# Kernel optimization log

Hardware: AMD Instinct MI355X
Metric: run time of the kernel (lower is better)

## Reference

```python
import jax, jax.numpy as jnp
import numpy as np

# Dimensions (see shape_source)
IN_VEC = 131072          # input_vector_size
NUM_CAPS = 512           # num_capsules (output capsules)
CAP_SIZE = 256           # capsule_size
RF_SIZE = 64             # receptive_field_size
RF_PER_CAP = CAP_SIZE // RF_SIZE        # 4
IN_CAPS = IN_VEC // CAP_SIZE            # 512 input_eff_capsules
CONN_P = 0.1             # connection_probability


def setup_inputs() -> dict:
    key = jax.random.key(0)
    kx, kc, kw = jax.random.split(key, 3)
    x = jax.random.normal(kx, (IN_VEC,), dtype=jnp.float32)
    # Sparse ScRRAMBLe routing tensor: mostly zeros, gated by connection probability.
    # Shape (input_eff_capsules, rf_per_cap_in, num_capsules, rf_per_cap_out) per einsum 'ijkl,ijm->klm'.
    Ci = (jax.random.uniform(kc, (IN_CAPS, RF_PER_CAP, NUM_CAPS, RF_PER_CAP)) < CONN_P).astype(jnp.float32)
    # glorot_normal over last two axes: fan_in = fan_out = RF_SIZE -> std = sqrt(2/(64+64)) = 0.125
    glorot_std = float(np.sqrt(2.0 / (RF_SIZE + RF_SIZE)))
    Wi = glorot_std * jax.random.normal(kw, (NUM_CAPS, RF_PER_CAP, RF_PER_CAP, RF_SIZE, RF_SIZE), dtype=jnp.float32)
    return {"x": x, "Ci": Ci, "Wi": Wi}


def reference(x, Ci, Wi):
    # x: (IN_VEC,) -> (input_eff_capsules, rf_per_cap, rf_size)
    x_reshaped = x.reshape(IN_CAPS, RF_PER_CAP, RF_SIZE)
    # Route input receptive fields to output capsule slots:
    # x_routed: (num_capsules, rf_per_cap, rf_size)
    x_routed = jnp.einsum('ijkl,ijm->klm', Ci, x_reshaped)
    # Per-capsule small batched transform:
    # y: (num_capsules, rf_per_cap, rf_size)
    y = jnp.einsum('ijklm,ikm->ijl', Wi, x_routed)
    return y
```

## Files before the change

kernel.cpp:

```cpp
#include <hip/hip_runtime.h>


typedef float f4 __attribute__((ext_vector_type(4)));

#define NCH 4

__global__ __launch_bounds__(256) void route_kernel(
    const float* __restrict__ x,
    const float* __restrict__ Ci,
    float* __restrict__ xr_part)
{
    const int iq  = blockIdx.x;
    const int c   = blockIdx.y;
    const int t   = threadIdx.x;
    const int il  = t >> 6;
    const int g   = (t >> 4) & 3;
    const int mq4 = t & 15;
    const int i   = (iq << 2) + il;

    const f4* __restrict__ Ci4 = (const f4*)Ci;
    const f4* __restrict__ x4  = (const f4*)x;

    __shared__ f4 part[1024];

    f4 a0 = {0.f,0.f,0.f,0.f};
    f4 a1 = {0.f,0.f,0.f,0.f};
    f4 a2 = {0.f,0.f,0.f,0.f};
    f4 a3 = {0.f,0.f,0.f,0.f};

    const int ijpc = 2048 / NCH;
    const int sub  = ijpc >> 2;
    const int base = c * ijpc + g * sub;
    #pragma unroll 4
    for (int it = 0; it < sub; ++it) {
        const int ij = base + it;
        const f4 c4 = Ci4[ij * 512 + i];
        const f4 xv = x4[(ij << 4) + mq4];
        a0 += c4.x * xv;
        a1 += c4.y * xv;
        a2 += c4.z * xv;
        a3 += c4.w * xv;
    }

    const int pb = ((g << 2) + il) << 2;
    part[(pb + 0) * 16 + mq4] = a0;
    part[(pb + 1) * 16 + mq4] = a1;
    part[(pb + 2) * 16 + mq4] = a2;
    part[(pb + 3) * 16 + mq4] = a3;
    __syncthreads();

    const int il2 = t >> 6;
    const int r   = (t >> 4) & 3;
    const int mm  = t & 15;
    f4 s = {0.f,0.f,0.f,0.f};
    #pragma unroll
    for (int gg = 0; gg < 4; ++gg)
        s += part[(((gg << 2) + il2) * 4 + r) * 16 + mm];

    f4* __restrict__ xp4 = (f4*)xr_part;
    xp4[(c * 512 + (iq << 2) + il2) * 64 + r * 16 + mm] = s;
}

__global__ __launch_bounds__(256, 2) void transform_kernel(
    const float* __restrict__ Wi,
    const float* __restrict__ xr_part,
    float* __restrict__ y)
{
    const int b    = blockIdx.x;
    const int i    = b >> 2;
    const int t    = threadIdx.x;
    const int lane = t & 63;
    const int w    = t >> 6;
    const int lq   = lane >> 4;
    const int m16  = lane & 15;
    const int lw   = w << 4;

    const f4* __restrict__ xp4 = (const f4*)xr_part;

    f4 xr0, xr1, xr2, xr3;
    {
        f4 tmp[8];
        #pragma unroll
        for (int ch = 0; ch < 2; ++ch)
            #pragma unroll
            for (int k = 0; k < 4; ++k)
                tmp[(ch << 2) + k] =
                    xp4[(((ch << 9) + i) << 6) + (k << 4) + m16];
        xr0 = tmp[0] + tmp[4];
        xr1 = tmp[1] + tmp[5];
        xr2 = tmp[2] + tmp[6];
        xr3 = tmp[3] + tmp[7];
        #pragma unroll
        for (int ch = 0; ch < 2; ++ch)
            #pragma unroll
            for (int k = 0; k < 4; ++k)
                tmp[(ch << 2) + k] =
                    xp4[((((ch + 2) << 9) + i) << 6) + (k << 4) + m16];
        xr0 += tmp[0] + tmp[4];
        xr1 += tmp[1] + tmp[5];
        xr2 += tmp[2] + tmp[6];
        xr3 += tmp[3] + tmp[7];
    }

    const float* wp = Wi + ((size_t)b << 14);

    f4 wv0, wv1, wv2,  wv3,  wv4,  wv5,  wv6,  wv7;
    f4 wv8, wv9, wv10, wv11, wv12, wv13, wv14, wv15;

#define WLOAD(n, c2, k)                                                      \
    {                                                                        \
        const float* ap = wp + ((k) << 12)                                   \
                        + ((lw + ((c2) << 2) + lq) << 6) + (m16 << 2);       \
        asm volatile("global_load_dwordx4 %0, %1, off"                       \
                     : "=v"(wv##n) : "v"(ap));                               \
    }

    WLOAD(0, 0, 0)  WLOAD(1, 0, 1)  WLOAD(2, 0, 2)  WLOAD(3, 0, 3)
    WLOAD(4, 1, 0)  WLOAD(5, 1, 1)  WLOAD(6, 1, 2)  WLOAD(7, 1, 3)
    WLOAD(8, 2, 0)  WLOAD(9, 2, 1)  WLOAD(10, 2, 2) WLOAD(11, 2, 3)
    WLOAD(12, 3, 0) WLOAD(13, 3, 1) WLOAD(14, 3, 2) WLOAD(15, 3, 3)
#undef WLOAD

    asm volatile("s_waitcnt vmcnt(0)" ::: "memory");
    __builtin_amdgcn_sched_barrier(0);

#define CONSUME(c2, wa, wb, wc, wd)                                          \
    {                                                                        \
        f4 s = wa * xr0 + wb * xr1 + wc * xr2 + wd * xr3;                    \
        float p = s.x + s.y + s.z + s.w;                                     \
        p += __shfl_xor(p, 1);                                               \
        p += __shfl_xor(p, 2);                                               \
        p += __shfl_xor(p, 4);                                               \
        p += __shfl_xor(p, 8);                                               \
        if (m16 == 0) y[(b << 6) + lw + ((c2) << 2) + lq] = p;               \
    }

    CONSUME(0, wv0,  wv1,  wv2,  wv3)
    CONSUME(1, wv4,  wv5,  wv6,  wv7)
    CONSUME(2, wv8,  wv9,  wv10, wv11)
    CONSUME(3, wv12, wv13, wv14, wv15)
#undef CONSUME
}

extern "C" void kernel_launch(void* const* d_in, const int* in_sizes, int n_in,
                              void* d_out, int out_size, void* d_ws, size_t ws_size,
                              hipStream_t stream) {
    const float* x  = (const float*)d_in[0];
    const float* Ci = (const float*)d_in[1];
    const float* Wi = (const float*)d_in[2];
    float* y  = (float*)d_out;
    float* xr = (float*)d_ws;

    route_kernel<<<dim3(128, NCH), 256, 0, stream>>>(x, Ci, xr);
    transform_kernel<<<2048, 256, 0, stream>>>(Wi, xr, y);
}
```

Baseline: 224.2 us.

## Process four capsule slices per block with double-buffered Wi loads

The transform kernel now launches one block per output capsule instead of per capsule-slice. Each block loads the routed input once and streams four 64KB Wi slices through two register buffers, issuing the next slice's loads before consuming the current one. This amortizes the xr_part reads and keeps memory loads in flight during compute. In exchange, register pressure roughly doubles and the grid shrinks to 512 blocks, which may lower occupancy on a large GPU.

```diff
diff --git a/kernel.cpp b/kernel.cpp
--- a/kernel.cpp
+++ b/kernel.cpp
@@ -66,8 +66,7 @@
     const float* __restrict__ xr_part,
     float* __restrict__ y)
 {
-    const int b    = blockIdx.x;
-    const int i    = b >> 2;
+    const int i    = blockIdx.x;
     const int t    = threadIdx.x;
     const int lane = t & 63;
     const int w    = t >> 6;
@@ -101,45 +100,70 @@
         xr2 += tmp[2] + tmp[6];
         xr3 += tmp[3] + tmp[7];
     }
-
-    const float* wp = Wi + ((size_t)b << 14);
-
-    f4 wv0, wv1, wv2,  wv3,  wv4,  wv5,  wv6,  wv7;
-    f4 wv8, wv9, wv10, wv11, wv12, wv13, wv14, wv15;
-
-#define WLOAD(n, c2, k)                                                      \
-    {                                                                        \
-        const float* ap = wp + ((k) << 12)                                   \
-                        + ((lw + ((c2) << 2) + lq) << 6) + (m16 << 2);       \
-        asm volatile("global_load_dwordx4 %0, %1, off"                       \
-                     : "=v"(wv##n) : "v"(ap));                               \
-    }
-
-    WLOAD(0, 0, 0)  WLOAD(1, 0, 1)  WLOAD(2, 0, 2)  WLOAD(3, 0, 3)
-    WLOAD(4, 1, 0)  WLOAD(5, 1, 1)  WLOAD(6, 1, 2)  WLOAD(7, 1, 3)
-    WLOAD(8, 2, 0)  WLOAD(9, 2, 1)  WLOAD(10, 2, 2) WLOAD(11, 2, 3)
-    WLOAD(12, 3, 0) WLOAD(13, 3, 1) WLOAD(14, 3, 2) WLOAD(15, 3, 3)
-#undef WLOAD
-
     asm volatile("s_waitcnt vmcnt(0)" ::: "memory");
     __builtin_amdgcn_sched_barrier(0);
 
-#define CONSUME(c2, wa, wb, wc, wd)                                          \
+    const float* wp = Wi + ((size_t)i << 16);
+
+    f4 a0, a1, a2,  a3,  a4,  a5,  a6,  a7;
+    f4 a8, a9, a10, a11, a12, a13, a14, a15;
+    f4 b0, b1, b2,  b3,  b4,  b5,  b6,  b7;
+    f4 b8, b9, b10, b11, b12, b13, b14, b15;
+
+#define WLOAD(var, j, c2, k)                                                 \
+    {                                                                        \
+        const float* ap = wp + ((j) << 14) + ((k) << 12)                     \
+                        + ((lw + ((c2) << 2) + lq) << 6) + (m16 << 2);       \
+        asm volatile("global_load_dwordx4 %0, %1, off"                       \
+                     : "=v"(var) : "v"(ap));                                 \
+    }
+
+#define ISSUE16(p, j)                                                        \
+    WLOAD(p##0, j, 0, 0)  WLOAD(p##1, j, 0, 1)                               \
+    WLOAD(p##2, j, 0, 2)  WLOAD(p##3, j, 0, 3)                               \
+    WLOAD(p##4, j, 1, 0)  WLOAD(p##5, j, 1, 1)                               \
+    WLOAD(p##6, j, 1, 2)  WLOAD(p##7, j, 1, 3)                               \
+    WLOAD(p##8, j, 2, 0)  WLOAD(p##9, j, 2, 1)                               \
+    WLOAD(p##10, j, 2, 2) WLOAD(p##11, j, 2, 3)                              \
+    WLOAD(p##12, j, 3, 0) WLOAD(p##13, j, 3, 1)                              \
+    WLOAD(p##14, j, 3, 2) WLOAD(p##15, j, 3, 3)
+
+#define CONS1(j, c2, wa, wb, wc, wd)                                         \
     {                                                                        \
         f4 s = wa * xr0 + wb * xr1 + wc * xr2 + wd * xr3;                    \
-        float p = s.x + s.y + s.z + s.w;                                     \
-        p += __shfl_xor(p, 1);                                               \
-        p += __shfl_xor(p, 2);                                               \
-        p += __shfl_xor(p, 4);                                               \
-        p += __shfl_xor(p, 8);                                               \
-        if (m16 == 0) y[(b << 6) + lw + ((c2) << 2) + lq] = p;               \
+        float pp = s.x + s.y + s.z + s.w;                                    \
+        pp += __shfl_xor(pp, 1);                                             \
+        pp += __shfl_xor(pp, 2);                                             \
+        pp += __shfl_xor(pp, 4);                                             \
+        pp += __shfl_xor(pp, 8);                                             \
+        if (m16 == 0)                                                        \
+            y[(((i << 2) + (j)) << 6) + lw + ((c2) << 2) + lq] = pp;         \
     }
 
-    CONSUME(0, wv0,  wv1,  wv2,  wv3)
-    CONSUME(1, wv4,  wv5,  wv6,  wv7)
-    CONSUME(2, wv8,  wv9,  wv10, wv11)
-    CONSUME(3, wv12, wv13, wv14, wv15)
-#undef CONSUME
+#define CONSUME16(p, j)                                                      \
+    CONS1(j, 0, p##0,  p##1,  p##2,  p##3)                                   \
+    CONS1(j, 1, p##4,  p##5,  p##6,  p##7)                                   \
+    CONS1(j, 2, p##8,  p##9,  p##10, p##11)                                  \
+    CONS1(j, 3, p##12, p##13, p##14, p##15)
+
+#define VMW16  asm volatile("s_waitcnt vmcnt(16)" ::: "memory");             \
+               __builtin_amdgcn_sched_barrier(0);
+#define VMW0   asm volatile("s_waitcnt vmcnt(0)" ::: "memory");              \
+               __builtin_amdgcn_sched_barrier(0);
+
+    ISSUE16(a, 0)
+    ISSUE16(b, 1)
+    VMW16  CONSUME16(a, 0)  ISSUE16(a, 2)
+    VMW16  CONSUME16(b, 1)  ISSUE16(b, 3)
+    VMW16  CONSUME16(a, 2)
+    VMW0   CONSUME16(b, 3)
+
+#undef WLOAD
+#undef ISSUE16
+#undef CONS1
+#undef CONSUME16
+#undef VMW16
+#undef VMW0
 }
 
 extern "C" void kernel_launch(void* const* d_in, const int* in_sizes, int n_in,
@@ -152,5 +176,5 @@
     float* xr = (float*)d_ws;
 
     route_kernel<<<dim3(128, NCH), 256, 0, stream>>>(x, Ci, xr);
-    transform_kernel<<<2048, 256, 0, stream>>>(Wi, xr, y);
+    transform_kernel<<<512, 256, 0, stream>>>(Wi, xr, y);
 }
```

Result: no change. 224.9 us (+0.3%).
